# Performance work log

Measured on AMD Instinct MI355X. Metric: run time of the kernel, lower is better.

Reference implementation:

```python
import jax, jax.numpy as jnp
import numpy as np

DIM = 4096
N_HEADS = 32
N_KV_HEADS = 8
HEAD_DIM = DIM // N_HEADS
N_REP = N_HEADS // N_KV_HEADS
SEQ = 2048
THETA = 10000.0


def _rope_tables(seq_len, dim, theta):
    angles = 1.0 / theta ** (np.arange(0, dim, 2, dtype=np.float32) / dim)
    emb = np.outer(np.arange(seq_len, dtype=np.float32), angles)
    emb = np.concatenate([emb, emb], axis=-1)  # [S, head_dim]
    return jnp.asarray(np.cos(emb)), jnp.asarray(np.sin(emb))


def setup_inputs() -> dict:
    key = jax.random.key(0)
    k0, k1, k2, k3, k4 = jax.random.split(key, 5)
    s = 0.02
    data = jax.random.normal(k0, (2, SEQ, DIM), dtype=jnp.float32)
    Wq = jax.random.normal(k1, (N_HEADS * HEAD_DIM, DIM), dtype=jnp.float32) * s
    Wk = jax.random.normal(k2, (N_KV_HEADS * HEAD_DIM, DIM), dtype=jnp.float32) * s
    Wv = jax.random.normal(k3, (N_KV_HEADS * HEAD_DIM, DIM), dtype=jnp.float32) * s
    Wo = jax.random.normal(k4, (DIM, N_HEADS * HEAD_DIM), dtype=jnp.float32) * s
    cos, sin = _rope_tables(SEQ, HEAD_DIM, THETA)
    mask = jnp.zeros((1,), dtype=jnp.float32)  # numel==1 -> causal
    return {"data": data, "Wq": Wq, "Wk": Wk, "Wv": Wv, "Wo": Wo,
            "cos": cos, "sin": sin, "mask": mask}


def _rotate_half(x):
    h = x.shape[-1] // 2
    return jnp.concatenate([-x[..., h:], x[..., :h]], axis=-1)


def reference(data, Wq, Wk, Wv, Wo, cos, sin, mask):
    B, S, _ = data.shape
    # QKV projections (torch Linear: y = x @ W^T)
    xq = jnp.einsum('bsd,od->bso', data, Wq).reshape(B, S, N_HEADS, HEAD_DIM).transpose(0, 2, 1, 3)
    xk = jnp.einsum('bsd,od->bso', data, Wk).reshape(B, S, N_KV_HEADS, HEAD_DIM).transpose(0, 2, 1, 3)
    xv = jnp.einsum('bsd,od->bso', data, Wv).reshape(B, S, N_KV_HEADS, HEAD_DIM).transpose(0, 2, 1, 3)
    # RoPE: broadcast [S, head_dim] over [B, H, S, head_dim]
    xq = xq * cos + _rotate_half(xq) * sin
    xk = xk * cos + _rotate_half(xk) * sin
    # repeat_kv (GQA): each kv head repeated N_REP times consecutively
    xk = jnp.repeat(xk, N_REP, axis=1)
    xv = jnp.repeat(xv, N_REP, axis=1)
    # causal SDPA
    scale = 1.0 / jnp.sqrt(jnp.asarray(HEAD_DIM, dtype=data.dtype))
    logits = jnp.einsum('bhqd,bhkd->bhqk', xq, xk) * scale
    causal = jnp.tril(jnp.ones((S, S), dtype=bool))
    logits = jnp.where(causal, logits, jnp.finfo(data.dtype).min)
    probs = jax.nn.softmax(logits, axis=-1)
    out = jnp.einsum('bhqk,bhkd->bhqd', probs, xv)
    out = out.transpose(0, 2, 1, 3).reshape(B, S, N_HEADS * HEAD_DIM)
    return jnp.einsum('bso,do->bsd', out, Wo)
```

## Files before the change

kernel.cpp:

```cpp
#include <hip/hip_runtime.h>

typedef __bf16 bf16x8 __attribute__((ext_vector_type(8)));
typedef __bf16 bf16x4 __attribute__((ext_vector_type(4)));
typedef float f32x4 __attribute__((ext_vector_type(4)));

__device__ __forceinline__ void gload_lds16(const __bf16* g, __bf16* l) {
    __builtin_amdgcn_global_load_lds((const __attribute__((address_space(1))) unsigned int*)g,
                                     (__attribute__((address_space(3))) unsigned int*)l,
                                     16, 0, 0);
}

template <int EPI>
__device__ __forceinline__ void store_tile(f32x4 (&acc)[4][4], void* Cp, __bf16* vt,
                                           int N, int m0, int n0, int wr, int wc,
                                           int lm, int lq) {
#pragma unroll
    for (int i = 0; i < 4; ++i) {
        int row0 = m0 + wr * 64 + i * 16 + lq * 4;
#pragma unroll
        for (int j = 0; j < 4; ++j) {
            int gc = n0 + wc * 64 + j * 16 + lm;
            if constexpr (EPI == 1) {
                float* C = (float*)Cp;
#pragma unroll
                for (int r = 0; r < 4; ++r) C[(size_t)(row0 + r) * N + gc] = acc[i][j][r];
            } else if constexpr (EPI == 0) {
                __bf16* C = (__bf16*)Cp;
#pragma unroll
                for (int r = 0; r < 4; ++r) C[(size_t)(row0 + r) * N + gc] = (__bf16)acc[i][j][r];
            } else {
                bool vpath = (EPI == 2) || (gc >= 1024);
                if (!vpath) {
                    __bf16* C = (__bf16*)Cp;
#pragma unroll
                    for (int r = 0; r < 4; ++r) C[(size_t)(row0 + r) * 1024 + gc] = (__bf16)acc[i][j][r];
                } else {
                    int dfull = (EPI == 2) ? gc : gc - 1024;
                    int kvh = dfull >> 7, d = dfull & 127;
                    int bq = row0 >> 11, s = row0 & 2047;
                    bf16x4 v;
#pragma unroll
                    for (int r = 0; r < 4; ++r) v[r] = (__bf16)acc[i][j][r];
                    *(bf16x4*)&vt[(((size_t)bq * 8 + kvh) * 128 + d) * 2048 + s] = v;
                }
            }
        }
    }
}

template <int EPI>
__global__ __launch_bounds__(256) void gemm_a16(const __bf16* __restrict__ A,
                                                const __bf16* __restrict__ B,
                                                void* __restrict__ Cp, __bf16* __restrict__ vt,
                                                int M, int N, int K) {
    __shared__ __bf16 As[4096];
    __shared__ __bf16 Bs[4096];
    const int tid = threadIdx.x;
    const int wave = tid >> 6, lane = tid & 63;
    const int lm = lane & 15, lq = lane >> 4;
    const int wr = wave >> 1, wc = wave & 1;
    const int n0 = blockIdx.x * 128, m0 = blockIdx.y * 128;

    f32x4 acc[4][4];
#pragma unroll
    for (int i = 0; i < 4; ++i)
#pragma unroll
        for (int j = 0; j < 4; ++j) acc[i][j] = (f32x4){0.f, 0.f, 0.f, 0.f};

    for (int k0 = 0; k0 < K; k0 += 32) {
        __syncthreads();
#pragma unroll
        for (int it = 0; it < 2; ++it) {
            int f = it * 256 + tid;
            int g = f >> 3, s = f & 7, sx = s ^ (g & 7);
            int row = g * 2 + (sx >> 2), kc = (sx & 3) * 8;
            gload_lds16(A + (size_t)(m0 + row) * K + k0 + kc, &As[f * 8]);
        }
#pragma unroll
        for (int it = 0; it < 2; ++it) {
            int f = it * 256 + tid;
            int g = f >> 3, s = f & 7, sx = s ^ (g & 7);
            int row = g * 2 + (sx >> 2), kc = (sx & 3) * 8;
            gload_lds16(B + (size_t)(n0 + row) * K + k0 + kc, &Bs[f * 8]);
        }
        __syncthreads();

        bf16x8 af[4], bfr[4];
#pragma unroll
        for (int i = 0; i < 4; ++i) {
            int rf = wr * 64 + i * 16 + lm;
            int g = rf >> 1, w = (rf & 1) * 4 + lq, s = w ^ (g & 7);
            af[i] = *(const bf16x8*)&As[g * 64 + s * 8];
        }
#pragma unroll
        for (int j = 0; j < 4; ++j) {
            int rf = wc * 64 + j * 16 + lm;
            int g = rf >> 1, w = (rf & 1) * 4 + lq, s = w ^ (g & 7);
            bfr[j] = *(const bf16x8*)&Bs[g * 64 + s * 8];
        }
#pragma unroll
        for (int i = 0; i < 4; ++i)
#pragma unroll
            for (int j = 0; j < 4; ++j)
                acc[i][j] = __builtin_amdgcn_mfma_f32_16x16x32_bf16(af[i], bfr[j], acc[i][j], 0, 0, 0);
    }
    store_tile<EPI>(acc, Cp, vt, N, m0, n0, wr, wc, lm, lq);
}

template <typename TA, int EPI>
__global__ __launch_bounds__(256) void gemm_bt(const TA* __restrict__ A,
                                               const float* __restrict__ W,
                                               void* __restrict__ Cp, __bf16* __restrict__ vt,
                                               int M, int N, int K) {
    __shared__ __bf16 Asl[128][40];
    __shared__ __bf16 Bsl[128][40];
    const int tid = threadIdx.x;
    const int wave = tid >> 6, lane = tid & 63;
    const int lm = lane & 15, lq = lane >> 4;
    const int wr = wave >> 1, wc = wave & 1;
    const int n0 = blockIdx.x * 128, m0 = blockIdx.y * 128;

    f32x4 acc[4][4];
#pragma unroll
    for (int i = 0; i < 4; ++i)
#pragma unroll
        for (int j = 0; j < 4; ++j) acc[i][j] = (f32x4){0.f, 0.f, 0.f, 0.f};

    for (int k0 = 0; k0 < K; k0 += 32) {
        __syncthreads();
        if constexpr (sizeof(TA) == 4) {
#pragma unroll
            for (int it = 0; it < 4; ++it) {
                int f = it * 1024 + tid * 4;
                int row = f >> 5, kc = f & 31;
                float4 a = *(const float4*)(const void*)(A + (size_t)(m0 + row) * K + k0 + kc);
                bf16x4 v;
                v[0] = (__bf16)a.x; v[1] = (__bf16)a.y; v[2] = (__bf16)a.z; v[3] = (__bf16)a.w;
                *(bf16x4*)&Asl[row][kc] = v;
            }
        } else {
#pragma unroll
            for (int it = 0; it < 2; ++it) {
                int f = it * 2048 + tid * 8;
                int row = f >> 5, kc = f & 31;
                *(bf16x8*)&Asl[row][kc] = *(const bf16x8*)(const void*)(A + (size_t)(m0 + row) * K + k0 + kc);
            }
        }
#pragma unroll
        for (int it = 0; it < 4; ++it) {
            int f = it * 1024 + tid * 4;
            int row = f >> 5, kc = f & 31;
            float4 a = *(const float4*)(const void*)(W + (size_t)(n0 + row) * K + k0 + kc);
            bf16x4 v;
            v[0] = (__bf16)a.x; v[1] = (__bf16)a.y; v[2] = (__bf16)a.z; v[3] = (__bf16)a.w;
            *(bf16x4*)&Bsl[row][kc] = v;
        }
        __syncthreads();

        bf16x8 af[4], bfr[4];
#pragma unroll
        for (int i = 0; i < 4; ++i) af[i] = *(const bf16x8*)&Asl[wr * 64 + i * 16 + lm][lq * 8];
#pragma unroll
        for (int j = 0; j < 4; ++j) bfr[j] = *(const bf16x8*)&Bsl[wc * 64 + j * 16 + lm][lq * 8];
#pragma unroll
        for (int i = 0; i < 4; ++i)
#pragma unroll
            for (int j = 0; j < 4; ++j)
                acc[i][j] = __builtin_amdgcn_mfma_f32_16x16x32_bf16(af[i], bfr[j], acc[i][j], 0, 0, 0);
    }
    store_tile<EPI>(acc, Cp, vt, N, m0, n0, wr, wc, lm, lq);
}

__global__ void cvt_kernel(const float* __restrict__ in, __bf16* __restrict__ out, int n8) {
    int i = blockIdx.x * 256 + threadIdx.x;
    if (i >= n8) return;
    const float4* p = (const float4*)in + (size_t)i * 2;
    float4 a = p[0], b = p[1];
    bf16x8 v;
    v[0] = (__bf16)a.x; v[1] = (__bf16)a.y; v[2] = (__bf16)a.z; v[3] = (__bf16)a.w;
    v[4] = (__bf16)b.x; v[5] = (__bf16)b.y; v[6] = (__bf16)b.z; v[7] = (__bf16)b.w;
    ((bf16x8*)out)[i] = v;
}

__global__ void rope_kernel(__bf16* __restrict__ X, const float* __restrict__ ct,
                            const float* __restrict__ st, int nheads, int total) {
    int idx = blockIdx.x * 256 + threadIdx.x;
    if (idx >= total) return;
    int d   = idx & 63;
    int hh  = (idx >> 6) % nheads;
    int row = idx / (64 * nheads);
    int s   = row & 2047;
    size_t base = (size_t)row * (nheads * 128) + hh * 128 + d;
    float x1 = (float)X[base], x2 = (float)X[base + 64];
    float c = ct[s * 128 + d], sn = st[s * 128 + d];
    X[base]      = (__bf16)(x1 * c - x2 * sn);
    X[base + 64] = (__bf16)(x2 * c + x1 * sn);
}

__global__ __launch_bounds__(256, 3) void attn2(const __bf16* __restrict__ Q,
                                                const __bf16* __restrict__ Kg,
                                                const __bf16* __restrict__ Vtg,
                                                __bf16* __restrict__ O) {
    __shared__ __bf16 Ks[32 * 136];
    __shared__ __bf16 Vt[128 * 40];
    __shared__ __bf16 Ps[4 * 32 * 40];

    const int tid = threadIdx.x;
    const int wave = tid >> 6, lane = tid & 63;
    const int lm = lane & 15, lq = lane >> 4;

    const int qt  = 63 - (blockIdx.x >> 4);
    const int bh  = blockIdx.x & 15;
    const int b   = bh >> 3, kvh = bh & 7;
    const int q0  = qt * 32;
    const int h   = kvh * 4 + wave;

    const __bf16* Qb = Q + ((size_t)b * 2048) * 4096 + h * 128;
    const __bf16* Kb = Kg + ((size_t)b * 2048) * 1024 + kvh * 128;
    const __bf16* Vb = Vtg + ((size_t)(b * 8 + kvh) * 128) * 2048;
    __bf16* Pw = &Ps[wave * 32 * 40];

    bf16x8 qf[2][4];
#pragma unroll
    for (int mf = 0; mf < 2; ++mf) {
        int row = q0 + mf * 16 + lm;
#pragma unroll
        for (int kk = 0; kk < 4; ++kk)
            qf[mf][kk] = *(const bf16x8*)(const void*)(Qb + (size_t)row * 4096 + kk * 32 + lq * 8);
    }

    f32x4 o[2][8];
#pragma unroll
    for (int mf = 0; mf < 2; ++mf)
#pragma unroll
        for (int dt = 0; dt < 8; ++dt) o[mf][dt] = (f32x4){0.f, 0.f, 0.f, 0.f};
    float m_i[2][4], l_i[2][4];
#pragma unroll
    for (int mf = 0; mf < 2; ++mf)
#pragma unroll
        for (int r = 0; r < 4; ++r) { m_i[mf][r] = -1e30f; l_i[mf][r] = 0.f; }

    const int nch = qt + 1;
    const float scale = 0.08838834764831845f;

    for (int ch = 0; ch < nch; ++ch) {
        const int j0 = ch * 32;
        __syncthreads();
#pragma unroll
        for (int it = 0; it < 2; ++it) {
            int f = it * 256 + tid;
            int row = f >> 4, c = (f & 15) * 8;
            *(bf16x8*)&Ks[row * 136 + c] =
                *(const bf16x8*)(const void*)(Kb + (size_t)(j0 + row) * 1024 + c);
        }
#pragma unroll
        for (int it = 0; it < 2; ++it) {
            int f = it * 256 + tid;
            int d = f >> 2, kc = (f & 3) * 8;
            *(bf16x8*)&Vt[d * 40 + kc] =
                *(const bf16x8*)(const void*)(Vb + (size_t)d * 2048 + j0 + kc);
        }
        __syncthreads();

        f32x4 st[2][2];
        st[0][0] = st[0][1] = st[1][0] = st[1][1] = (f32x4){0.f, 0.f, 0.f, 0.f};
#pragma unroll
        for (int kk = 0; kk < 4; ++kk) {
            bf16x8 k0f = *(const bf16x8*)&Ks[lm * 136 + kk * 32 + lq * 8];
            bf16x8 k1f = *(const bf16x8*)&Ks[(16 + lm) * 136 + kk * 32 + lq * 8];
            st[0][0] = __builtin_amdgcn_mfma_f32_16x16x32_bf16(qf[0][kk], k0f, st[0][0], 0, 0, 0);
            st[0][1] = __builtin_amdgcn_mfma_f32_16x16x32_bf16(qf[0][kk], k1f, st[0][1], 0, 0, 0);
            st[1][0] = __builtin_amdgcn_mfma_f32_16x16x32_bf16(qf[1][kk], k0f, st[1][0], 0, 0, 0);
            st[1][1] = __builtin_amdgcn_mfma_f32_16x16x32_bf16(qf[1][kk], k1f, st[1][1], 0, 0, 0);
        }

        const bool diag = (ch == nch - 1);
#pragma unroll
        for (int mf = 0; mf < 2; ++mf) {
#pragma unroll
            for (int r = 0; r < 4; ++r) {
                float v0 = st[mf][0][r] * scale;
                float v1 = st[mf][1][r] * scale;
                if (diag) {
                    int row_loc = mf * 16 + lq * 4 + r;
                    if (lm > row_loc)      v0 = -1e30f;
                    if (16 + lm > row_loc) v1 = -1e30f;
                }
                float mx = fmaxf(v0, v1);
                mx = fmaxf(mx, __shfl_xor(mx, 1));
                mx = fmaxf(mx, __shfl_xor(mx, 2));
                mx = fmaxf(mx, __shfl_xor(mx, 4));
                mx = fmaxf(mx, __shfl_xor(mx, 8));
                float mn = fmaxf(m_i[mf][r], mx);
                float al = __expf(m_i[mf][r] - mn);
                float p0 = __expf(v0 - mn);
                float p1 = __expf(v1 - mn);
                float sm = p0 + p1;
                sm += __shfl_xor(sm, 1);
                sm += __shfl_xor(sm, 2);
                sm += __shfl_xor(sm, 4);
                sm += __shfl_xor(sm, 8);
                l_i[mf][r] = al * l_i[mf][r] + sm;
                m_i[mf][r] = mn;
#pragma unroll
                for (int dt = 0; dt < 8; ++dt) o[mf][dt][r] *= al;
                int ql = mf * 16 + lq * 4 + r;
                Pw[ql * 40 + lm]      = (__bf16)p0;
                Pw[ql * 40 + 16 + lm] = (__bf16)p1;
            }
        }
        __builtin_amdgcn_s_waitcnt(0xC07F);

        bf16x8 pf0 = *(const bf16x8*)&Pw[lm * 40 + lq * 8];
        bf16x8 pf1 = *(const bf16x8*)&Pw[(16 + lm) * 40 + lq * 8];
#pragma unroll
        for (int dt = 0; dt < 8; ++dt) {
            bf16x8 vf = *(const bf16x8*)&Vt[(dt * 16 + lm) * 40 + lq * 8];
            o[0][dt] = __builtin_amdgcn_mfma_f32_16x16x32_bf16(pf0, vf, o[0][dt], 0, 0, 0);
            o[1][dt] = __builtin_amdgcn_mfma_f32_16x16x32_bf16(pf1, vf, o[1][dt], 0, 0, 0);
        }
    }

#pragma unroll
    for (int mf = 0; mf < 2; ++mf) {
#pragma unroll
        for (int r = 0; r < 4; ++r) {
            int row = q0 + mf * 16 + lq * 4 + r;
            float inv = 1.0f / l_i[mf][r];
#pragma unroll
            for (int dt = 0; dt < 8; ++dt)
                O[((size_t)b * 2048 + row) * 4096 + h * 128 + dt * 16 + lm] =
                    (__bf16)(o[mf][dt][r] * inv);
        }
    }
}

extern "C" void kernel_launch(void* const* d_in, const int* in_sizes, int n_in,
                              void* d_out, int out_size, void* d_ws, size_t ws_size,
                              hipStream_t stream) {
    const float* data = (const float*)d_in[0];
    const float* Wq   = (const float*)d_in[1];
    const float* Wk   = (const float*)d_in[2];
    const float* Wv   = (const float*)d_in[3];
    const float* Wo   = (const float*)d_in[4];
    const float* cost = (const float*)d_in[5];
    const float* sint = (const float*)d_in[6];
    float* out = (float*)d_out;

    char* ws = (char*)d_ws;
    __bf16* qb   = (__bf16*)(ws);
    __bf16* kb   = (__bf16*)(ws + 33554432);
    __bf16* vt   = (__bf16*)(ws + 41943040);
    __bf16* attn = (__bf16*)(ws + 50331648);
    __bf16* dbf  = (__bf16*)(ws + 83886080);
    __bf16* wbuf = (__bf16*)(ws + 117440512);
    const bool fast = ws_size >= 150994944ULL;

    if (fast) {
        cvt_kernel<<<8192, 256, 0, stream>>>(data, dbf, 2097152);
        cvt_kernel<<<8192, 256, 0, stream>>>(Wq, wbuf, 2097152);
        gemm_a16<0><<<dim3(32, 32), 256, 0, stream>>>(dbf, wbuf, qb, nullptr, 4096, 4096, 4096);
        cvt_kernel<<<2048, 256, 0, stream>>>(Wk, wbuf, 524288);
        cvt_kernel<<<2048, 256, 0, stream>>>(Wv, wbuf + 4194304, 524288);
        gemm_a16<3><<<dim3(16, 32), 256, 0, stream>>>(dbf, wbuf, kb, vt, 4096, 2048, 4096);
    } else {
        gemm_bt<float, 0><<<dim3(32, 32), 256, 0, stream>>>(data, Wq, qb, nullptr, 4096, 4096, 4096);
        gemm_bt<float, 0><<<dim3(8, 32), 256, 0, stream>>>(data, Wk, kb, nullptr, 4096, 1024, 4096);
        gemm_bt<float, 2><<<dim3(8, 32), 256, 0, stream>>>(data, Wv, nullptr, vt, 4096, 1024, 4096);
    }
    rope_kernel<<<(4096 * 32 * 64) / 256, 256, 0, stream>>>(qb, cost, sint, 32, 4096 * 32 * 64);
    rope_kernel<<<(4096 * 8 * 64) / 256, 256, 0, stream>>>(kb, cost, sint, 8, 4096 * 8 * 64);
    attn2<<<1024, 256, 0, stream>>>(qb, kb, vt, attn);
    if (fast) {
        cvt_kernel<<<8192, 256, 0, stream>>>(Wo, wbuf, 2097152);
        gemm_a16<1><<<dim3(32, 32), 256, 0, stream>>>(attn, wbuf, out, nullptr, 4096, 4096, 4096);
    } else {
        gemm_bt<__bf16, 1><<<dim3(32, 32), 256, 0, stream>>>(attn, Wo, out, nullptr, 4096, 4096, 4096);
    }
}
```

Measured before the change: 991.6 us.

## Widen attention KV tile to 64 with async LDS loads and lazy rescale

```diff
diff --git a/kernel.cpp b/kernel.cpp
--- a/kernel.cpp
+++ b/kernel.cpp
@@ -197,13 +197,13 @@
     X[base + 64] = (__bf16)(x2 * c + x1 * sn);
 }
 
-__global__ __launch_bounds__(256, 3) void attn2(const __bf16* __restrict__ Q,
+__global__ __launch_bounds__(256, 3) void attn3(const __bf16* __restrict__ Q,
                                                 const __bf16* __restrict__ Kg,
                                                 const __bf16* __restrict__ Vtg,
                                                 __bf16* __restrict__ O) {
-    __shared__ __bf16 Ks[32 * 136];
-    __shared__ __bf16 Vt[128 * 40];
-    __shared__ __bf16 Ps[4 * 32 * 40];
+    __shared__ __bf16 Ks[64 * 128];
+    __shared__ __bf16 Vs[128 * 64];
+    __shared__ __bf16 Ps[4 * 32 * 72];
 
     const int tid = threadIdx.x;
     const int wave = tid >> 6, lane = tid & 63;
@@ -218,15 +218,20 @@
     const __bf16* Qb = Q + ((size_t)b * 2048) * 4096 + h * 128;
     const __bf16* Kb = Kg + ((size_t)b * 2048) * 1024 + kvh * 128;
     const __bf16* Vb = Vtg + ((size_t)(b * 8 + kvh) * 128) * 2048;
-    __bf16* Pw = &Ps[wave * 32 * 40];
-
+    __bf16* Pw = &Ps[wave * 32 * 72];
+
+    const float sc2 = 0.08838834764831845f * 1.4426950408889634f;
     bf16x8 qf[2][4];
 #pragma unroll
     for (int mf = 0; mf < 2; ++mf) {
         int row = q0 + mf * 16 + lm;
 #pragma unroll
-        for (int kk = 0; kk < 4; ++kk)
-            qf[mf][kk] = *(const bf16x8*)(const void*)(Qb + (size_t)row * 4096 + kk * 32 + lq * 8);
+        for (int kk = 0; kk < 4; ++kk) {
+            bf16x8 v = *(const bf16x8*)(const void*)(Qb + (size_t)row * 4096 + kk * 32 + lq * 8);
+#pragma unroll
+            for (int e = 0; e < 8; ++e) v[e] = (__bf16)((float)v[e] * sc2);
+            qf[mf][kk] = v;
+        }
     }
 
     f32x4 o[2][8];
@@ -240,38 +245,46 @@
 #pragma unroll
         for (int r = 0; r < 4; ++r) { m_i[mf][r] = -1e30f; l_i[mf][r] = 0.f; }
 
-    const int nch = qt + 1;
-    const float scale = 0.08838834764831845f;
+    const int nch = (qt + 2) >> 1;
 
     for (int ch = 0; ch < nch; ++ch) {
-        const int j0 = ch * 32;
-        __syncthreads();
-#pragma unroll
-        for (int it = 0; it < 2; ++it) {
-            int f = it * 256 + tid;
-            int row = f >> 4, c = (f & 15) * 8;
-            *(bf16x8*)&Ks[row * 136 + c] =
-                *(const bf16x8*)(const void*)(Kb + (size_t)(j0 + row) * 1024 + c);
-        }
-#pragma unroll
-        for (int it = 0; it < 2; ++it) {
-            int f = it * 256 + tid;
-            int d = f >> 2, kc = (f & 3) * 8;
-            *(bf16x8*)&Vt[d * 40 + kc] =
-                *(const bf16x8*)(const void*)(Vb + (size_t)d * 2048 + j0 + kc);
-        }
-        __syncthreads();
-
-        f32x4 st[2][2];
-        st[0][0] = st[0][1] = st[1][0] = st[1][1] = (f32x4){0.f, 0.f, 0.f, 0.f};
+        const int j0 = ch * 64;
+        __syncthreads();
+#pragma unroll
+        for (int it = 0; it < 4; ++it) {
+            int p = it * 256 + tid;
+            int g = p >> 3, s = (p & 7) ^ (g & 7);
+            int L = g * 8 + s, row = L >> 4, c = L & 15;
+            gload_lds16(Kb + (size_t)(j0 + row) * 1024 + c * 8, &Ks[p * 8]);
+        }
+#pragma unroll
+        for (int it = 0; it < 4; ++it) {
+            int p = it * 256 + tid;
+            int d = p >> 3, c = (p & 7) ^ (d & 7);
+            gload_lds16(Vb + (size_t)d * 2048 + j0 + c * 8, &Vs[p * 8]);
+        }
+        __syncthreads();
+
+        f32x4 st[2][4];
+#pragma unroll
+        for (int mf = 0; mf < 2; ++mf)
+#pragma unroll
+            for (int nc = 0; nc < 4; ++nc) st[mf][nc] = (f32x4){0.f, 0.f, 0.f, 0.f};
 #pragma unroll
         for (int kk = 0; kk < 4; ++kk) {
-            bf16x8 k0f = *(const bf16x8*)&Ks[lm * 136 + kk * 32 + lq * 8];
-            bf16x8 k1f = *(const bf16x8*)&Ks[(16 + lm) * 136 + kk * 32 + lq * 8];
-            st[0][0] = __builtin_amdgcn_mfma_f32_16x16x32_bf16(qf[0][kk], k0f, st[0][0], 0, 0, 0);
-            st[0][1] = __builtin_amdgcn_mfma_f32_16x16x32_bf16(qf[0][kk], k1f, st[0][1], 0, 0, 0);
-            st[1][0] = __builtin_amdgcn_mfma_f32_16x16x32_bf16(qf[1][kk], k0f, st[1][0], 0, 0, 0);
-            st[1][1] = __builtin_amdgcn_mfma_f32_16x16x32_bf16(qf[1][kk], k1f, st[1][1], 0, 0, 0);
+            bf16x8 kf[4];
+#pragma unroll
+            for (int nc = 0; nc < 4; ++nc) {
+                int L = (nc * 16 + lm) * 16 + kk * 4 + lq;
+                int g = L >> 3;
+                int p = g * 8 + ((L & 7) ^ (g & 7));
+                kf[nc] = *(const bf16x8*)&Ks[p * 8];
+            }
+#pragma unroll
+            for (int mf = 0; mf < 2; ++mf)
+#pragma unroll
+                for (int nc = 0; nc < 4; ++nc)
+                    st[mf][nc] = __builtin_amdgcn_mfma_f32_16x16x32_bf16(qf[mf][kk], kf[nc], st[mf][nc], 0, 0, 0);
         }
 
         const bool diag = (ch == nch - 1);
@@ -279,45 +292,52 @@
         for (int mf = 0; mf < 2; ++mf) {
 #pragma unroll
             for (int r = 0; r < 4; ++r) {
-                float v0 = st[mf][0][r] * scale;
-                float v1 = st[mf][1][r] * scale;
+                float v0 = st[mf][0][r], v1 = st[mf][1][r], v2 = st[mf][2][r], v3 = st[mf][3][r];
                 if (diag) {
-                    int row_loc = mf * 16 + lq * 4 + r;
-                    if (lm > row_loc)      v0 = -1e30f;
-                    if (16 + lm > row_loc) v1 = -1e30f;
+                    int rel = (q0 - j0) + mf * 16 + lq * 4 + r;
+                    if (lm      > rel) v0 = -1e30f;
+                    if (lm + 16 > rel) v1 = -1e30f;
+                    if (lm + 32 > rel) v2 = -1e30f;
+                    if (lm + 48 > rel) v3 = -1e30f;
                 }
-                float mx = fmaxf(v0, v1);
+                float mx = fmaxf(fmaxf(v0, v1), fmaxf(v2, v3));
                 mx = fmaxf(mx, __shfl_xor(mx, 1));
                 mx = fmaxf(mx, __shfl_xor(mx, 2));
                 mx = fmaxf(mx, __shfl_xor(mx, 4));
                 mx = fmaxf(mx, __shfl_xor(mx, 8));
-                float mn = fmaxf(m_i[mf][r], mx);
-                float al = __expf(m_i[mf][r] - mn);
-                float p0 = __expf(v0 - mn);
-                float p1 = __expf(v1 - mn);
-                float sm = p0 + p1;
-                sm += __shfl_xor(sm, 1);
-                sm += __shfl_xor(sm, 2);
-                sm += __shfl_xor(sm, 4);
-                sm += __shfl_xor(sm, 8);
-                l_i[mf][r] = al * l_i[mf][r] + sm;
-                m_i[mf][r] = mn;
-#pragma unroll
-                for (int dt = 0; dt < 8; ++dt) o[mf][dt][r] *= al;
+                float mo = m_i[mf][r];
+                float mn = fmaxf(mo, mx);
+                if (__any(mx > mo)) {
+                    float al = exp2f(mo - mn);
+                    l_i[mf][r] *= al;
+                    m_i[mf][r] = mn;
+#pragma unroll
+                    for (int dt = 0; dt < 8; ++dt) o[mf][dt][r] *= al;
+                }
+                float p0 = exp2f(v0 - mn), p1 = exp2f(v1 - mn);
+                float p2 = exp2f(v2 - mn), p3 = exp2f(v3 - mn);
+                l_i[mf][r] += (p0 + p1) + (p2 + p3);
                 int ql = mf * 16 + lq * 4 + r;
-                Pw[ql * 40 + lm]      = (__bf16)p0;
-                Pw[ql * 40 + 16 + lm] = (__bf16)p1;
+                Pw[ql * 72 + lm]      = (__bf16)p0;
+                Pw[ql * 72 + lm + 16] = (__bf16)p1;
+                Pw[ql * 72 + lm + 32] = (__bf16)p2;
+                Pw[ql * 72 + lm + 48] = (__bf16)p3;
             }
         }
         __builtin_amdgcn_s_waitcnt(0xC07F);
 
-        bf16x8 pf0 = *(const bf16x8*)&Pw[lm * 40 + lq * 8];
-        bf16x8 pf1 = *(const bf16x8*)&Pw[(16 + lm) * 40 + lq * 8];
-#pragma unroll
-        for (int dt = 0; dt < 8; ++dt) {
-            bf16x8 vf = *(const bf16x8*)&Vt[(dt * 16 + lm) * 40 + lq * 8];
-            o[0][dt] = __builtin_amdgcn_mfma_f32_16x16x32_bf16(pf0, vf, o[0][dt], 0, 0, 0);
-            o[1][dt] = __builtin_amdgcn_mfma_f32_16x16x32_bf16(pf1, vf, o[1][dt], 0, 0, 0);
+#pragma unroll
+        for (int kvf = 0; kvf < 2; ++kvf) {
+            bf16x8 pf0 = *(const bf16x8*)&Pw[lm * 72 + kvf * 32 + lq * 8];
+            bf16x8 pf1 = *(const bf16x8*)&Pw[(16 + lm) * 72 + kvf * 32 + lq * 8];
+#pragma unroll
+            for (int dt = 0; dt < 8; ++dt) {
+                int d = dt * 16 + lm;
+                int p = d * 8 + ((kvf * 4 + lq) ^ (d & 7));
+                bf16x8 vf = *(const bf16x8*)&Vs[p * 8];
+                o[0][dt] = __builtin_amdgcn_mfma_f32_16x16x32_bf16(pf0, vf, o[0][dt], 0, 0, 0);
+                o[1][dt] = __builtin_amdgcn_mfma_f32_16x16x32_bf16(pf1, vf, o[1][dt], 0, 0, 0);
+            }
         }
     }
 
@@ -325,8 +345,13 @@
     for (int mf = 0; mf < 2; ++mf) {
 #pragma unroll
         for (int r = 0; r < 4; ++r) {
+            float l = l_i[mf][r];
+            l += __shfl_xor(l, 1);
+            l += __shfl_xor(l, 2);
+            l += __shfl_xor(l, 4);
+            l += __shfl_xor(l, 8);
+            float inv = 1.0f / l;
             int row = q0 + mf * 16 + lq * 4 + r;
-            float inv = 1.0f / l_i[mf][r];
 #pragma unroll
             for (int dt = 0; dt < 8; ++dt)
                 O[((size_t)b * 2048 + row) * 4096 + h * 128 + dt * 16 + lm] =
@@ -370,7 +395,7 @@
     }
     rope_kernel<<<(4096 * 32 * 64) / 256, 256, 0, stream>>>(qb, cost, sint, 32, 4096 * 32 * 64);
     rope_kernel<<<(4096 * 8 * 64) / 256, 256, 0, stream>>>(kb, cost, sint, 8, 4096 * 8 * 64);
-    attn2<<<1024, 256, 0, stream>>>(qb, kb, vt, attn);
+    attn3<<<1024, 256, 0, stream>>>(qb, kb, vt, attn);
     if (fast) {
         cvt_kernel<<<8192, 256, 0, stream>>>(Wo, wbuf, 2097152);
         gemm_a16<1><<<dim3(32, 32), 256, 0, stream>>>(attn, wbuf, out, nullptr, 4096, 4096, 4096);
```

After: 1.080 ms. 1.09x slower.
